# Kernel optimization log

Hardware: AMD Instinct MI355X
Metric: run time of the kernel (lower is better)

## Reference

```python
import jax, jax.numpy as jnp
import numpy as np

LENGTH = 4096
BATCH = 4096
N_OBS = 2


def setup_inputs() -> dict:
    key = jax.random.key(0)
    k1, k2, k3 = jax.random.split(key, 3)
    # Scale potentials down: the original chain performs no message
    # normalization, so we keep per-step log-growth tiny to avoid overflow.
    j = jax.random.normal(k1, (), dtype=jnp.float32) * 0.01
    b = jax.random.normal(k2, (N_OBS,), dtype=jnp.float32) * 0.01
    observations = jax.random.randint(k3, (BATCH, LENGTH), 0, N_OBS, dtype=jnp.int32)
    return {"j": j, "b": b, "observations": observations}


def reference(j, b, observations):
    # Max-product belief propagation on a binary-state chain CRF,
    # vectorized over the batch and scanned over the chain length.
    B, L = observations.shape
    values = jnp.array([-0.5, 0.5], dtype=jnp.float32)          # states {0,1} - 0.5
    pairs = values[:, None] * values[None, :]                    # [2,2] outer product
    psi = jnp.exp(j * pairs)                                     # [2,2] pairwise potential
    # Unary potentials phi[b_idx, i, s] = exp(b[obs] * values[s])
    phi = jnp.exp(b[observations][..., None] * values)           # [B,L,2]
    phi_tm = jnp.transpose(phi, (1, 0, 2))                       # time-major [L,B,2]

    def step(msg, phi_t):
        # msg_new[k] = max_l phi_t[l] * msg[l] * psi[k,l]
        x = phi_t * msg                                          # [B,2]
        new = jnp.max(x[:, None, :] * psi[None, :, :], axis=2)   # [B,2]
        return new, new

    ones = jnp.ones((B, 2), dtype=phi.dtype)
    # Forward messages: column 0 is ones, column t uses obs[0..t-1]
    _, fwd_msgs = jax.lax.scan(step, ones, phi_tm[:-1])          # [L-1,B,2]
    forward = jnp.concatenate([ones[None], fwd_msgs], axis=0)    # [L,B,2]
    # Backward messages: iterate i = L-1 .. 1, last column is ones
    _, bwd_msgs = jax.lax.scan(step, ones, phi_tm[1:][::-1])     # [L-1,B,2]
    backward = jnp.concatenate([bwd_msgs[::-1], ones[None]], axis=0)  # [L,B,2]

    beliefs = phi_tm * forward * backward                        # [L,B,2]
    return jnp.transpose(beliefs, (1, 2, 0))                     # [B,2,L]
```

## Files before the change

### kernel.cpp

```cpp
#include <hip/hip_runtime.h>
#include <hip/hip_bf16.h>
#include <math.h>

#define LENGTH 4096
#define BATCH  4096
#define CHUNK  8
#define NTHR   512
#define NWAVE  (NTHR / 64)

typedef float vf4 __attribute__((ext_vector_type(4)));

__device__ __forceinline__ void mp_compose(
    float a00, float a01, float a10, float a11,
    float b00, float b01, float b10, float b11,
    float& d00, float& d01, float& d10, float& d11) {
  d00 = fmaxf(a00 + b00, a01 + b10);
  d01 = fmaxf(a00 + b01, a01 + b11);
  d10 = fmaxf(a10 + b00, a11 + b10);
  d11 = fmaxf(a10 + b01, a11 + b11);
}

__device__ __forceinline__ void mp_step(
    float& f00, float& f01, float& f10, float& f11, float ui, float q) {
  float a0l0 = f00 - ui, a1l0 = f10 + ui;
  float a0l1 = f01 - ui, a1l1 = f11 + ui;
  float n00 = fmaxf(a0l0 + q, a1l0 - q);
  float n10 = fmaxf(a0l0 - q, a1l0 + q);
  float n01 = fmaxf(a0l1 + q, a1l1 - q);
  float n11 = fmaxf(a0l1 - q, a1l1 + q);
  f00 = n00; f01 = n01; f10 = n10; f11 = n11;
}

__global__ __launch_bounds__(NTHR, 6) void chain_bp_kernel(
    const float* __restrict__ jp, const float* __restrict__ bp,
    const int* __restrict__ obs, float* __restrict__ out) {
  const int row  = blockIdx.x;
  const int tid  = threadIdx.x;
  const int lane = tid & 63;
  const int wv   = tid >> 6;

  const float j  = jp[0];
  const float q  = 0.25f * j;
  const float u0 = 0.5f * bp[0];
  const float u1 = 0.5f * bp[1];
  const float wb = -fabsf(q);

  const int t0 = tid * CHUNK;
  const int4* op = reinterpret_cast<const int4*>(obs + (size_t)row * LENGTH + t0);
  float u[CHUNK];
#pragma unroll
  for (int v = 0; v < CHUNK / 4; ++v) {
    int4 o = op[v];
    u[4 * v + 0] = o.x ? u1 : u0;
    u[4 * v + 1] = o.y ? u1 : u0;
    u[4 * v + 2] = o.z ? u1 : u0;
    u[4 * v + 3] = o.w ? u1 : u0;
  }

  float l00 = -u[0] + q, l01 = u[0] - q, l10 = -u[0] - q, l11 = u[0] + q;
  float h00 = -u[4] + q, h01 = u[4] - q, h10 = -u[4] - q, h11 = u[4] + q;
#pragma unroll
  for (int i = 1; i < 4; ++i) {
    mp_step(l00, l01, l10, l11, u[i], q);
    mp_step(h00, h01, h10, h11, u[4 + i], q);
  }
  float f00, f01, f10, f11;
  mp_compose(h00, h01, h10, h11, l00, l01, l10, l11, f00, f01, f10, f11);

  float x00 = f00, x01 = f01, x10 = f10, x11 = f11;
#pragma unroll
  for (int d = 1; d < 64; d <<= 1) {
    float p00 = __shfl_up(x00, d), p01 = __shfl_up(x01, d);
    float p10 = __shfl_up(x10, d), p11 = __shfl_up(x11, d);
    if (lane >= d) {
      float n00, n01, n10, n11;
      mp_compose(x00, x01, x10, x11, p00, p01, p10, p11, n00, n01, n10, n11);
      x00 = n00; x01 = n01; x10 = n10; x11 = n11;
    }
  }
  float y00 = f00, y01 = f10, y10 = f01, y11 = f11;
#pragma unroll
  for (int d = 1; d < 64; d <<= 1) {
    float p00 = __shfl_down(y00, d), p01 = __shfl_down(y01, d);
    float p10 = __shfl_down(y10, d), p11 = __shfl_down(y11, d);
    if (lane + d < 64) {
      float n00, n01, n10, n11;
      mp_compose(y00, y01, y10, y11, p00, p01, p10, p11, n00, n01, n10, n11);
      y00 = n00; y01 = n01; y10 = n10; y11 = n11;
    }
  }

  __shared__ float smp[NWAVE][4];
  __shared__ float sms[NWAVE][4];
  if (lane == 63) { smp[wv][0] = x00; smp[wv][1] = x01; smp[wv][2] = x10; smp[wv][3] = x11; }
  if (lane == 0)  { sms[wv][0] = y00; sms[wv][1] = y01; sms[wv][2] = y10; sms[wv][3] = y11; }
  __syncthreads();

  float fh0 = 0.f, fh1 = 0.f;
  for (int k = 0; k < wv; ++k) {
    float m00 = smp[k][0], m01 = smp[k][1], m10 = smp[k][2], m11 = smp[k][3];
    float n0 = fmaxf(m00 + fh0, m01 + fh1);
    float n1 = fmaxf(m10 + fh0, m11 + fh1);
    fh0 = n0; fh1 = n1;
  }
  float wt0 = wb, wt1 = wb;
  for (int k = NWAVE - 1; k > wv; --k) {
    float m00 = sms[k][0], m01 = sms[k][1], m10 = sms[k][2], m11 = sms[k][3];
    float n0 = fmaxf(m00 + wt0, m01 + wt1);
    float n1 = fmaxf(m10 + wt0, m11 + wt1);
    wt0 = n0; wt1 = n1;
  }

  float z0 = fmaxf(x00 + fh0, x01 + fh1);
  float z1 = fmaxf(x10 + fh0, x11 + fh1);
  float zp0 = __shfl_up(z0, 1), zp1 = __shfl_up(z1, 1);
  float fi0 = (lane == 0) ? fh0 : zp0;
  float fi1 = (lane == 0) ? fh1 : zp1;

  float yv0 = fmaxf(y00 + wt0, y01 + wt1);
  float yv1 = fmaxf(y10 + wt0, y11 + wt1);
  float yn0 = __shfl_down(yv0, 1), yn1 = __shfl_down(yv1, 1);
  float wc0 = (lane == 63) ? wt0 : yn0;
  float wc1 = (lane == 63) ? wt1 : yn1;
  float g0 = fmaxf(q + wc0, -q + wc1);
  float g1 = fmaxf(-q + wc0, q + wc1);

  float b0[CHUNK], b1[CHUNK];
  b0[CHUNK - 1] = g0; b1[CHUNK - 1] = g1;
#pragma unroll
  for (int i = CHUNK - 1; i > 0; --i) {
    float ui = u[i];
    float a0 = b0[i] - ui;
    float a1 = b1[i] + ui;
    b0[i - 1] = fmaxf(a0 + q, a1 - q);
    b1[i - 1] = fmaxf(a0 - q, a1 + q);
  }

  float* outp = out + (size_t)row * (2 * LENGTH) + t0;
  float fw0 = fi0, fw1 = fi1;
  vf4 acc0, acc1;
#pragma unroll
  for (int i = 0; i < CHUNK; ++i) {
    float ui = u[i];
    float e0 = __expf(-ui + fw0 + b0[i]);
    float e1 = __expf( ui + fw1 + b1[i]);
    acc0[i & 3] = e0;
    acc1[i & 3] = e1;
    if ((i & 3) == 3) {
      __builtin_nontemporal_store(acc0, reinterpret_cast<vf4*>(outp + (i - 3)));
      __builtin_nontemporal_store(acc1, reinterpret_cast<vf4*>(outp + LENGTH + (i - 3)));
    }
    float a0 = fw0 - ui, a1 = fw1 + ui;
    float n0 = fmaxf(a0 + q, a1 - q);
    float n1 = fmaxf(a0 - q, a1 + q);
    fw0 = n0; fw1 = n1;
  }
}

extern "C" void kernel_launch(void* const* d_in, const int* in_sizes, int n_in,
                              void* d_out, int out_size, void* d_ws, size_t ws_size,
                              hipStream_t stream) {
  const float* jp  = (const float*)d_in[0];
  const float* bp  = (const float*)d_in[1];
  const int*   obs = (const int*)d_in[2];
  float* out = (float*)d_out;

  chain_bp_kernel<<<BATCH, NTHR, 0, stream>>>(jp, bp, obs, out);
}
```

Before: 223.1 us.

## Use 16-element chunks with shared-memory LUT of 8-step transfer matrices

Doubles the per-thread chunk to 16 and halves the block to 256 threads. Each thread's 16-step max-plus transfer matrix now comes from a 256-entry shared lookup table of 8-step compositions indexed by observation bits, replacing the sequential per-step scan. The forward and backward wave scans are interleaved in one loop, and stores are batched at the end as regular rather than nontemporal writes. The cost is extra LDS traffic, two block barriers and more registers per thread.

Result: faster. 202.0 us (-9.5%).

```diff
diff --git a/kernel.cpp b/kernel.cpp
--- a/kernel.cpp
+++ b/kernel.cpp
@@ -4,8 +4,8 @@
 
 #define LENGTH 4096
 #define BATCH  4096
-#define CHUNK  8
-#define NTHR   512
+#define CHUNK  16
+#define NTHR   256
 #define NWAVE  (NTHR / 64)
 
 typedef float vf4 __attribute__((ext_vector_type(4)));
@@ -31,7 +31,7 @@
   f00 = n00; f01 = n01; f10 = n10; f11 = n11;
 }
 
-__global__ __launch_bounds__(NTHR, 6) void chain_bp_kernel(
+__global__ __launch_bounds__(NTHR, 4) void chain_bp_kernel(
     const float* __restrict__ jp, const float* __restrict__ bp,
     const int* __restrict__ obs, float* __restrict__ out) {
   const int row  = blockIdx.x;
@@ -45,53 +45,70 @@
   const float u1 = 0.5f * bp[1];
   const float wb = -fabsf(q);
 
-  const int t0 = tid * CHUNK;
-  const int4* op = reinterpret_cast<const int4*>(obs + (size_t)row * LENGTH + t0);
+  __shared__ float l00[256], l01[256], l10[256], l11[256];
+  __shared__ float lut4[16][4];
+  __shared__ float smp[NWAVE][4];
+  __shared__ float sms[NWAVE][4];
+
+  const int t0i = tid * CHUNK;
+  const int4* op = reinterpret_cast<const int4*>(obs + (size_t)row * LENGTH + t0i);
+  int4 o0 = op[0], o1 = op[1], o2 = op[2], o3 = op[3];
   float u[CHUNK];
+  u[0]=o0.x?u1:u0; u[1]=o0.y?u1:u0; u[2]=o0.z?u1:u0; u[3]=o0.w?u1:u0;
+  u[4]=o1.x?u1:u0; u[5]=o1.y?u1:u0; u[6]=o1.z?u1:u0; u[7]=o1.w?u1:u0;
+  u[8]=o2.x?u1:u0; u[9]=o2.y?u1:u0; u[10]=o2.z?u1:u0; u[11]=o2.w?u1:u0;
+  u[12]=o3.x?u1:u0; u[13]=o3.y?u1:u0; u[14]=o3.z?u1:u0; u[15]=o3.w?u1:u0;
+  int idxlo = o0.x | (o0.y<<1) | (o0.z<<2) | (o0.w<<3)
+            | (o1.x<<4) | (o1.y<<5) | (o1.z<<6) | (o1.w<<7);
+  int idxhi = o2.x | (o2.y<<1) | (o2.z<<2) | (o2.w<<3)
+            | (o3.x<<4) | (o3.y<<5) | (o3.z<<6) | (o3.w<<7);
+
+  if (tid < 16) {
+    float ua = (tid & 1) ? u1 : u0;
+    float f00 = -ua + q, f01 = ua - q, f10 = -ua - q, f11 = ua + q;
 #pragma unroll
-  for (int v = 0; v < CHUNK / 4; ++v) {
-    int4 o = op[v];
-    u[4 * v + 0] = o.x ? u1 : u0;
-    u[4 * v + 1] = o.y ? u1 : u0;
-    u[4 * v + 2] = o.z ? u1 : u0;
-    u[4 * v + 3] = o.w ? u1 : u0;
+    for (int k = 1; k < 4; ++k)
+      mp_step(f00, f01, f10, f11, ((tid >> k) & 1) ? u1 : u0, q);
+    lut4[tid][0] = f00; lut4[tid][1] = f01; lut4[tid][2] = f10; lut4[tid][3] = f11;
+  }
+  __syncthreads();
+  {
+    int hi = tid >> 4, lo = tid & 15;
+    float a00 = lut4[hi][0], a01 = lut4[hi][1], a10 = lut4[hi][2], a11 = lut4[hi][3];
+    float c00 = lut4[lo][0], c01 = lut4[lo][1], c10 = lut4[lo][2], c11 = lut4[lo][3];
+    float d00, d01, d10, d11;
+    mp_compose(a00, a01, a10, a11, c00, c01, c10, c11, d00, d01, d10, d11);
+    l00[tid] = d00; l01[tid] = d01; l10[tid] = d10; l11[tid] = d11;
+  }
+  __syncthreads();
+
+  float f00, f01, f10, f11;
+  {
+    float a00 = l00[idxhi], a01 = l01[idxhi], a10 = l10[idxhi], a11 = l11[idxhi];
+    float c00 = l00[idxlo], c01 = l01[idxlo], c10 = l10[idxlo], c11 = l11[idxlo];
+    mp_compose(a00, a01, a10, a11, c00, c01, c10, c11, f00, f01, f10, f11);
   }
 
-  float l00 = -u[0] + q, l01 = u[0] - q, l10 = -u[0] - q, l11 = u[0] + q;
-  float h00 = -u[4] + q, h01 = u[4] - q, h10 = -u[4] - q, h11 = u[4] + q;
-#pragma unroll
-  for (int i = 1; i < 4; ++i) {
-    mp_step(l00, l01, l10, l11, u[i], q);
-    mp_step(h00, h01, h10, h11, u[4 + i], q);
-  }
-  float f00, f01, f10, f11;
-  mp_compose(h00, h01, h10, h11, l00, l01, l10, l11, f00, f01, f10, f11);
-
   float x00 = f00, x01 = f01, x10 = f10, x11 = f11;
-#pragma unroll
-  for (int d = 1; d < 64; d <<= 1) {
-    float p00 = __shfl_up(x00, d), p01 = __shfl_up(x01, d);
-    float p10 = __shfl_up(x10, d), p11 = __shfl_up(x11, d);
-    if (lane >= d) {
-      float n00, n01, n10, n11;
-      mp_compose(x00, x01, x10, x11, p00, p01, p10, p11, n00, n01, n10, n11);
-      x00 = n00; x01 = n01; x10 = n10; x11 = n11;
-    }
-  }
   float y00 = f00, y01 = f10, y10 = f01, y11 = f11;
 #pragma unroll
   for (int d = 1; d < 64; d <<= 1) {
-    float p00 = __shfl_down(y00, d), p01 = __shfl_down(y01, d);
-    float p10 = __shfl_down(y10, d), p11 = __shfl_down(y11, d);
+    float px00 = __shfl_up(x00, d), px01 = __shfl_up(x01, d);
+    float px10 = __shfl_up(x10, d), px11 = __shfl_up(x11, d);
+    float py00 = __shfl_down(y00, d), py01 = __shfl_down(y01, d);
+    float py10 = __shfl_down(y10, d), py11 = __shfl_down(y11, d);
+    if (lane >= d) {
+      float n00, n01, n10, n11;
+      mp_compose(x00, x01, x10, x11, px00, px01, px10, px11, n00, n01, n10, n11);
+      x00 = n00; x01 = n01; x10 = n10; x11 = n11;
+    }
     if (lane + d < 64) {
       float n00, n01, n10, n11;
-      mp_compose(y00, y01, y10, y11, p00, p01, p10, p11, n00, n01, n10, n11);
+      mp_compose(y00, y01, y10, y11, py00, py01, py10, py11, n00, n01, n10, n11);
       y00 = n00; y01 = n01; y10 = n10; y11 = n11;
     }
   }
 
-  __shared__ float smp[NWAVE][4];
-  __shared__ float sms[NWAVE][4];
   if (lane == 63) { smp[wv][0] = x00; smp[wv][1] = x01; smp[wv][2] = x10; smp[wv][3] = x11; }
   if (lane == 0)  { sms[wv][0] = y00; sms[wv][1] = y01; sms[wv][2] = y10; sms[wv][3] = y11; }
   __syncthreads();
@@ -125,35 +142,42 @@
   float g0 = fmaxf(q + wc0, -q + wc1);
   float g1 = fmaxf(-q + wc0, q + wc1);
 
-  float b0[CHUNK], b1[CHUNK];
-  b0[CHUNK - 1] = g0; b1[CHUNK - 1] = g1;
+  float e0v[CHUNK], e1v[CHUNK];
+  {
+    float r0 = g0, r1 = g1;
+    e0v[CHUNK - 1] = r0 - u[CHUNK - 1];
+    e1v[CHUNK - 1] = r1 + u[CHUNK - 1];
 #pragma unroll
-  for (int i = CHUNK - 1; i > 0; --i) {
-    float ui = u[i];
-    float a0 = b0[i] - ui;
-    float a1 = b1[i] + ui;
-    b0[i - 1] = fmaxf(a0 + q, a1 - q);
-    b1[i - 1] = fmaxf(a0 - q, a1 + q);
+    for (int i = CHUNK - 1; i > 0; --i) {
+      float a0 = r0 - u[i], a1 = r1 + u[i];
+      r0 = fmaxf(a0 + q, a1 - q);
+      r1 = fmaxf(a0 - q, a1 + q);
+      e0v[i - 1] = r0 - u[i - 1];
+      e1v[i - 1] = r1 + u[i - 1];
+    }
   }
 
-  float* outp = out + (size_t)row * (2 * LENGTH) + t0;
   float fw0 = fi0, fw1 = fi1;
-  vf4 acc0, acc1;
 #pragma unroll
   for (int i = 0; i < CHUNK; ++i) {
     float ui = u[i];
-    float e0 = __expf(-ui + fw0 + b0[i]);
-    float e1 = __expf( ui + fw1 + b1[i]);
-    acc0[i & 3] = e0;
-    acc1[i & 3] = e1;
-    if ((i & 3) == 3) {
-      __builtin_nontemporal_store(acc0, reinterpret_cast<vf4*>(outp + (i - 3)));
-      __builtin_nontemporal_store(acc1, reinterpret_cast<vf4*>(outp + LENGTH + (i - 3)));
-    }
+    e0v[i] = __expf(e0v[i] + fw0);
+    e1v[i] = __expf(e1v[i] + fw1);
     float a0 = fw0 - ui, a1 = fw1 + ui;
-    float n0 = fmaxf(a0 + q, a1 - q);
-    float n1 = fmaxf(a0 - q, a1 + q);
-    fw0 = n0; fw1 = n1;
+    fw0 = fmaxf(a0 + q, a1 - q);
+    fw1 = fmaxf(a0 - q, a1 + q);
+  }
+
+  float* outp = out + (size_t)row * (2 * LENGTH) + t0i;
+#pragma unroll
+  for (int v = 0; v < 4; ++v) {
+    vf4 s0 = {e0v[4 * v], e0v[4 * v + 1], e0v[4 * v + 2], e0v[4 * v + 3]};
+    *reinterpret_cast<vf4*>(outp + 4 * v) = s0;
+  }
+#pragma unroll
+  for (int v = 0; v < 4; ++v) {
+    vf4 s1 = {e1v[4 * v], e1v[4 * v + 1], e1v[4 * v + 2], e1v[4 * v + 3]};
+    *reinterpret_cast<vf4*>(outp + LENGTH + 4 * v) = s1;
   }
 }
 
```
